# Kernel optimization log

Measured on AMD Instinct MI355X. Metric: run time of the kernel, lower is better.

Reference implementation:

```python
import jax, jax.numpy as jnp
import numpy as np

N, C, H, W = 8, 256, 128, 128
HW = H * W
NB = 20            # boxes per image
TEMP = 0.5
RATIO = 1.0
IMG_H, IMG_W = 800.0, 800.0  # img_metas[i]['img_shape']


def setup_inputs() -> dict:
    key = jax.random.key(0)
    k1, k2, k3 = jax.random.split(key, 3)
    preds_S = jax.random.normal(k1, (HW, N, C), dtype=jnp.float32)
    preds_T = jax.random.normal(k2, (HW, N, C), dtype=jnp.float32)
    # boxes: random corner pairs in image coords, sorted so x1<=x2, y1<=y2
    u = jax.random.uniform(k3, (N, NB, 4), dtype=jnp.float32)
    x1 = jnp.minimum(u[..., 0], u[..., 2]) * IMG_W
    x2 = jnp.maximum(u[..., 0], u[..., 2]) * IMG_W
    y1 = jnp.minimum(u[..., 1], u[..., 3]) * IMG_H
    y2 = jnp.maximum(u[..., 1], u[..., 3]) * IMG_H
    gt_bboxes = jnp.stack([x1, y1, x2, y2], axis=-1)  # (N, NB, 4)
    return {"preds_S": preds_S, "preds_T": preds_T, "gt_bboxes": gt_bboxes}


def get_attention(preds, temp):
    # preds: (N, C, H, W)
    value = jnp.abs(preds)
    fea_map = value.mean(axis=1)                                   # (N, H, W)
    S_att = (H * W) * jax.nn.softmax((fea_map / temp).reshape(N, -1), axis=1)
    S_att = S_att.reshape(N, H, W)
    channel_map = value.mean(axis=(2, 3))                          # (N, C)
    C_att = C * jax.nn.softmax(channel_map / temp, axis=1)
    return S_att, C_att


def build_masks(gt_bboxes):
    # boxes scaled to feature grid (same math as torch loop, vectorized)
    wmin = jnp.floor(gt_bboxes[..., 0] / IMG_W * W).astype(jnp.int32)  # (N, NB)
    wmax = jnp.ceil(gt_bboxes[..., 2] / IMG_W * W).astype(jnp.int32)
    hmin = jnp.floor(gt_bboxes[..., 1] / IMG_H * H).astype(jnp.int32)
    hmax = jnp.ceil(gt_bboxes[..., 3] / IMG_H * H).astype(jnp.int32)
    area = 1.0 / (hmax + 1 - hmin).astype(jnp.float32) / (wmax + 1 - wmin).astype(jnp.float32)
    hh = jnp.arange(H)[None, None, :, None]
    ww = jnp.arange(W)[None, None, None, :]
    inside = ((hh >= hmin[:, :, None, None]) & (hh <= hmax[:, :, None, None]) &
              (ww >= wmin[:, :, None, None]) & (ww <= wmax[:, :, None, None]))  # (N, NB, H, W)
    # per-box max-scatter == max over boxes of (area where inside else 0)
    Mask_fg = jnp.max(jnp.where(inside, area[:, :, None, None], 0.0), axis=1)  # (N, H, W)
    Mask_bg = (Mask_fg <= 0).astype(jnp.float32)
    s = Mask_bg.sum(axis=(1, 2), keepdims=True)
    Mask_bg = jnp.where(s > 0, Mask_bg / s, Mask_bg)
    return Mask_fg, Mask_bg


def reference(preds_S, preds_T, gt_bboxes):
    # attention from DETACHED teacher features (preds_T.detach() in torch)
    pT_det = jax.lax.stop_gradient(preds_T)
    pT_new = pT_det.reshape(H, W, N, C).transpose(2, 3, 0, 1)  # (N, C, H, W)
    S_t, C_t = get_attention(pT_new, TEMP)

    Mask_fg, Mask_bg = build_masks(gt_bboxes)

    # flatten to the (HW, bs, .) layout of get_fea_loss
    flat = lambda m: m.transpose(1, 2, 0).reshape(HW, N, 1)
    S_t_f = flat(S_t)
    Mfg_f = flat(Mask_fg)
    Mbg_f = flat(Mask_bg)
    C_t_f = C_t[None]  # (1, bs, c) broadcast

    w = jnp.sqrt(S_t_f) * jnp.sqrt(C_t_f)
    fea_t = preds_T * w
    fea_s = preds_S * w
    diff = jnp.abs(fea_s - fea_t)
    fg_loss = jnp.sum(diff * jnp.sqrt(Mfg_f)) / HW
    bg_loss = jnp.sum(diff * jnp.sqrt(Mbg_f)) / HW
    return (fg_loss + bg_loss) * RATIO
```

## Files before the change

### kernel.cpp

```cpp
#include <hip/hip_runtime.h>

#define N_   8
#define C_   256
#define H_   128
#define W_   128
#define HW_  16384
#define NB_  20
constexpr float TEMP  = 0.5f;
constexpr float IMG_W = 800.0f;
constexpr float IMG_H = 800.0f;

__device__ __forceinline__ float waveReduceSum(float v) {
    v += __shfl_xor(v, 32, 64);
    v += __shfl_xor(v, 16, 64);
    v += __shfl_xor(v, 8, 64);
    v += __shfl_xor(v, 4, 64);
    v += __shfl_xor(v, 2, 64);
    v += __shfl_xor(v, 1, 64);
    return v;
}

__global__ __launch_bounds__(256, 4) void k_stats(const float* __restrict__ pT,
                                                  float* __restrict__ chan_part,
                                                  float* __restrict__ fea_sum,
                                                  float* __restrict__ smax_part) {
    const int n     = blockIdx.x & 7;
    const int chunk = blockIdx.x >> 3;
    const int wave  = threadIdx.x >> 6;
    const int lane  = threadIdx.x & 63;
    const int hw0   = chunk * 64 + wave * 16;

    float4 cacc = make_float4(0.f, 0.f, 0.f, 0.f);
    float vmax = 0.f;
    #pragma unroll
    for (int g = 0; g < 4; ++g) {
        const int r = hw0 + g * 4;
        float p[4];
        #pragma unroll
        for (int j = 0; j < 4; ++j) {
            const float4 v = *(const float4*)(pT + ((size_t)((r + j) * N_ + n)) * C_ + lane * 4);
            const float ax = fabsf(v.x), ay = fabsf(v.y), az = fabsf(v.z), aw = fabsf(v.w);
            cacc.x += ax; cacc.y += ay; cacc.z += az; cacc.w += aw;
            p[j] = ax + ay + az + aw;
        }
        float a01 = (lane & 32) ? p[1] : p[0];
        float b01 = (lane & 32) ? p[0] : p[1];
        const float u01 = a01 + __shfl_xor(b01, 32, 64);
        float a23 = (lane & 32) ? p[3] : p[2];
        float b23 = (lane & 32) ? p[2] : p[3];
        const float u23 = a23 + __shfl_xor(b23, 32, 64);
        float aq = (lane & 16) ? u23 : u01;
        float bq = (lane & 16) ? u01 : u23;
        float u = aq + __shfl_xor(bq, 16, 64);
        u += __shfl_xor(u, 8, 64);
        u += __shfl_xor(u, 4, 64);
        u += __shfl_xor(u, 2, 64);
        u += __shfl_xor(u, 1, 64);
        vmax = fmaxf(vmax, u);
        if ((lane & 15) == 0) {
            const int q = lane >> 4;
            const int row = ((q & 1) << 1) | (q >> 1);
            fea_sum[n * HW_ + r + row] = u;
        }
    }
    vmax = fmaxf(vmax, __shfl_xor(vmax, 16, 64));
    vmax = fmaxf(vmax, __shfl_xor(vmax, 32, 64));

    __shared__ float lds[4][C_];
    __shared__ float wmax[4];
    if (lane == 0) wmax[wave] = vmax;
    ((float4*)lds[wave])[lane] = cacc;
    __syncthreads();
    const int c = threadIdx.x;
    chan_part[((size_t)(n * 256 + chunk)) * C_ + c] =
        lds[0][c] + lds[1][c] + lds[2][c] + lds[3][c];
    if (threadIdx.x == 0)
        smax_part[n * 256 + chunk] =
            fmaxf(fmaxf(wmax[0], wmax[1]), fmaxf(wmax[2], wmax[3]));
}

__global__ __launch_bounds__(256) void k_soft(const float* __restrict__ fea_sum,
                                              const float* __restrict__ chan_part,
                                              const float* __restrict__ smax_part,
                                              const float* __restrict__ gt,
                                              float* __restrict__ sden_part,
                                              float* __restrict__ bg_part,
                                              float* __restrict__ Mfg,
                                              float* __restrict__ stats,
                                              float* __restrict__ B) {
    const int n   = blockIdx.x >> 3;
    const int sub = blockIdx.x & 7;
    const int tid = threadIdx.x;
    __shared__ float red[256];

    red[tid] = smax_part[n * 256 + tid];
    __syncthreads();
    for (int s = 128; s > 0; s >>= 1) { if (tid < s) red[tid] = fmaxf(red[tid], red[tid + s]); __syncthreads(); }
    const float sm = red[0] * (1.0f / (C_ * TEMP));
    __syncthreads();

    float acc = 0.f;
    const int base = n * HW_ + sub * 2048;
    #pragma unroll
    for (int k = 0; k < 8; ++k)
        acc += expf(fea_sum[base + k * 256 + tid] * (1.0f / (C_ * TEMP)) - sm);
    red[tid] = acc; __syncthreads();
    for (int s = 128; s > 0; s >>= 1) { if (tid < s) red[tid] += red[tid + s]; __syncthreads(); }
    if (tid == 0) sden_part[n * 8 + sub] = red[0];
    __syncthreads();

    float fg[8] = {0.f, 0.f, 0.f, 0.f, 0.f, 0.f, 0.f, 0.f};
    for (int b = 0; b < NB_; ++b) {
        const float* bx = gt + ((size_t)n * NB_ + b) * 4;
        const float x1 = bx[0], y1 = bx[1], x2 = bx[2], y2 = bx[3];
        const int wmin = (int)floorf(x1 / IMG_W * (float)W_);
        const int wmax = (int)ceilf (x2 / IMG_W * (float)W_);
        const int hmin = (int)floorf(y1 / IMG_H * (float)H_);
        const int hmax = (int)ceilf (y2 / IMG_H * (float)H_);
        const float area = 1.0f / (float)(hmax + 1 - hmin) / (float)(wmax + 1 - wmin);
        #pragma unroll
        for (int k = 0; k < 8; ++k) {
            const int hw = sub * 2048 + k * 256 + tid;
            const int h = hw >> 7, w = hw & 127;
            if (h >= hmin && h <= hmax && w >= wmin && w <= wmax)
                fg[k] = fmaxf(fg[k], area);
        }
    }
    float bgc = 0.f;
    #pragma unroll
    for (int k = 0; k < 8; ++k) {
        const int hw = sub * 2048 + k * 256 + tid;
        Mfg[n * HW_ + hw] = fg[k];
        bgc += (fg[k] <= 0.f) ? 1.f : 0.f;
    }
    red[tid] = bgc; __syncthreads();
    for (int s = 128; s > 0; s >>= 1) { if (tid < s) red[tid] += red[tid + s]; __syncthreads(); }
    if (tid == 0) bg_part[n * 8 + sub] = red[0];
    if (tid == 0 && sub == 0) stats[n] = sm;

    if (sub != 0) return;
    __syncthreads();

    float cs = 0.f;
    #pragma unroll 4
    for (int k2 = 0; k2 < 256; ++k2)
        cs += chan_part[((size_t)(n * 256 + k2)) * C_ + tid];
    const float lc = cs * (1.0f / (HW_ * TEMP));
    red[tid] = lc; __syncthreads();
    for (int s = 128; s > 0; s >>= 1) { if (tid < s) red[tid] = fmaxf(red[tid], red[tid + s]); __syncthreads(); }
    const float cmax = red[0]; __syncthreads();
    const float e = expf(lc - cmax);
    red[tid] = e; __syncthreads();
    for (int s = 128; s > 0; s >>= 1) { if (tid < s) red[tid] += red[tid + s]; __syncthreads(); }
    B[n * C_ + tid] = sqrtf((float)C_ * e / red[0]);
}

__global__ __launch_bounds__(256, 4) void k_main(const float* __restrict__ pS,
                                                 const float* __restrict__ pT,
                                                 const float* __restrict__ fea_sum,
                                                 const float* __restrict__ Mfg,
                                                 const float* __restrict__ bg_part,
                                                 const float* __restrict__ stats,
                                                 const float* __restrict__ sden_part,
                                                 const float* __restrict__ B,
                                                 float* __restrict__ partials) {
    const int wave = threadIdx.x >> 6, lane = threadIdx.x & 63;
    const int wg   = blockIdx.x * 4 + wave;
    const int n    = wg & 7;
    const int widx = wg >> 3;
    const int hw0  = widx * 16;
    const float sm = stats[n];
    float sden = 0.f, bgs = 0.f;
    #pragma unroll
    for (int j = 0; j < 8; ++j) { sden += sden_part[n * 8 + j]; bgs += bg_part[n * 8 + j]; }
    const float bginv = (bgs > 0.f) ? 1.0f / bgs : 1.0f;
    const float4 B4 = *(const float4*)(B + n * C_ + lane * 4);
    float acc = 0.f;
    #pragma unroll 4
    for (int i = 0; i < 16; ++i) {
        const int hw = hw0 + i;
        const float fs = fea_sum[n * HW_ + hw];
        const float fg = Mfg[n * HW_ + hw];
        const float S_att = (float)HW_ * expf(fs * (1.0f / (C_ * TEMP)) - sm) / sden;
        const float bg = (fg <= 0.f) ? bginv : 0.f;
        const float a_row = sqrtf(S_att) * (sqrtf(fg) + sqrtf(bg)) * (1.0f / (float)HW_);
        const size_t off = ((size_t)(hw * N_ + n)) * C_ + lane * 4;
        const float4 sv = *(const float4*)(pS + off);
        const float4 tv = *(const float4*)(pT + off);
        const float part = fabsf(sv.x - tv.x) * B4.x + fabsf(sv.y - tv.y) * B4.y +
                           fabsf(sv.z - tv.z) * B4.z + fabsf(sv.w - tv.w) * B4.w;
        acc += a_row * part;
    }
    acc = waveReduceSum(acc);
    __shared__ float red[4];
    if (lane == 0) red[wave] = acc;
    __syncthreads();
    if (threadIdx.x == 0) partials[blockIdx.x] = red[0] + red[1] + red[2] + red[3];
}

__global__ __launch_bounds__(256) void k_final(const float* __restrict__ partials,
                                               float* __restrict__ out) {
    float a = 0.f;
    for (int i = threadIdx.x; i < 2048; i += 256) a += partials[i];
    __shared__ float red[256];
    red[threadIdx.x] = a; __syncthreads();
    for (int s = 128; s > 0; s >>= 1) { if (threadIdx.x < s) red[threadIdx.x] += red[threadIdx.x + s]; __syncthreads(); }
    if (threadIdx.x == 0) out[0] = red[0];
}

extern "C" void kernel_launch(void* const* d_in, const int* in_sizes, int n_in,
                              void* d_out, int out_size, void* d_ws, size_t ws_size,
                              hipStream_t stream) {
    const float* pS = (const float*)d_in[0];
    const float* pT = (const float*)d_in[1];
    const float* gt = (const float*)d_in[2];
    float* ws = (float*)d_ws;

    float* chan_part = ws;
    float* smax_part = chan_part + 524288;
    float* sden_part = smax_part + 2048;
    float* bg_part   = sden_part + 64;
    float* stats     = bg_part + 64;
    float* fea_sum   = ws + 528384;
    float* Mfg       = fea_sum + N_ * HW_;
    float* B         = Mfg + N_ * HW_;
    float* partials  = B + N_ * C_;

    k_stats<<<2048, 256, 0, stream>>>(pT, chan_part, fea_sum, smax_part);
    k_soft <<<64,   256, 0, stream>>>(fea_sum, chan_part, smax_part, gt,
                                      sden_part, bg_part, Mfg, stats, B);
    k_main <<<2048, 256, 0, stream>>>(pS, pT, fea_sum, Mfg, bg_part, stats,
                                      sden_part, B, partials);
    k_final<<<1,    256, 0, stream>>>(partials, (float*)d_out);
}
```

Before: 315.0 us.

## Batch loads up front in stats/main kernels and precompute per-row weights in new kernel

k_stats now issues all 16 float4 loads of teacher data before reducing them, which raises memory-level parallelism. A new k_A kernel precomputes the per-pixel weight (spatial attention times mask terms) into a workspace array. k_main then loads one weight per lane and broadcasts it with shuffles, and it issues 8 rows of student and teacher loads at a time. This removes exp/sqrt work from the bandwidth-bound main loop, at the cost of more registers, an extra small launch and an extra workspace buffer.

Result: no change. 315.6 us (+0.2%).

```diff
diff --git a/kernel.cpp b/kernel.cpp
--- a/kernel.cpp
+++ b/kernel.cpp
@@ -30,6 +30,11 @@
     const int lane  = threadIdx.x & 63;
     const int hw0   = chunk * 64 + wave * 16;
 
+    float4 v[16];
+    #pragma unroll
+    for (int j = 0; j < 16; ++j)
+        v[j] = *(const float4*)(pT + ((size_t)((hw0 + j) * N_ + n)) * C_ + lane * 4);
+
     float4 cacc = make_float4(0.f, 0.f, 0.f, 0.f);
     float vmax = 0.f;
     #pragma unroll
@@ -38,8 +43,8 @@
         float p[4];
         #pragma unroll
         for (int j = 0; j < 4; ++j) {
-            const float4 v = *(const float4*)(pT + ((size_t)((r + j) * N_ + n)) * C_ + lane * 4);
-            const float ax = fabsf(v.x), ay = fabsf(v.y), az = fabsf(v.z), aw = fabsf(v.w);
+            const float4 w = v[g * 4 + j];
+            const float ax = fabsf(w.x), ay = fabsf(w.y), az = fabsf(w.z), aw = fabsf(w.w);
             cacc.x += ax; cacc.y += ay; cacc.z += az; cacc.w += aw;
             p[j] = ax + ay + az + aw;
         }
@@ -155,41 +160,58 @@
     B[n * C_ + tid] = sqrtf((float)C_ * e / red[0]);
 }
 
+__global__ __launch_bounds__(256) void k_A(const float* __restrict__ fea_sum,
+                                           const float* __restrict__ Mfg,
+                                           const float* __restrict__ sden_part,
+                                           const float* __restrict__ bg_part,
+                                           const float* __restrict__ stats,
+                                           float* __restrict__ A) {
+    const int n   = blockIdx.x >> 3;
+    const int sub = blockIdx.x & 7;
+    const int tid = threadIdx.x;
+    const float sm = stats[n];
+    float sden = 0.f, bgs = 0.f;
+    #pragma unroll
+    for (int j = 0; j < 8; ++j) { sden += sden_part[n * 8 + j]; bgs += bg_part[n * 8 + j]; }
+    const float bginv = (bgs > 0.f) ? 1.0f / bgs : 1.0f;
+    #pragma unroll
+    for (int k = 0; k < 8; ++k) {
+        const int hw = sub * 2048 + k * 256 + tid;
+        const float fs = fea_sum[n * HW_ + hw];
+        const float fg = Mfg[n * HW_ + hw];
+        const float S_att = (float)HW_ * expf(fs * (1.0f / (C_ * TEMP)) - sm) / sden;
+        const float bg = (fg <= 0.f) ? bginv : 0.f;
+        A[n * HW_ + hw] = sqrtf(S_att) * (sqrtf(fg) + sqrtf(bg)) * (1.0f / (float)HW_);
+    }
+}
+
 __global__ __launch_bounds__(256, 4) void k_main(const float* __restrict__ pS,
                                                  const float* __restrict__ pT,
-                                                 const float* __restrict__ fea_sum,
-                                                 const float* __restrict__ Mfg,
-                                                 const float* __restrict__ bg_part,
-                                                 const float* __restrict__ stats,
-                                                 const float* __restrict__ sden_part,
+                                                 const float* __restrict__ A,
                                                  const float* __restrict__ B,
                                                  float* __restrict__ partials) {
     const int wave = threadIdx.x >> 6, lane = threadIdx.x & 63;
     const int wg   = blockIdx.x * 4 + wave;
     const int n    = wg & 7;
-    const int widx = wg >> 3;
-    const int hw0  = widx * 16;
-    const float sm = stats[n];
-    float sden = 0.f, bgs = 0.f;
-    #pragma unroll
-    for (int j = 0; j < 8; ++j) { sden += sden_part[n * 8 + j]; bgs += bg_part[n * 8 + j]; }
-    const float bginv = (bgs > 0.f) ? 1.0f / bgs : 1.0f;
+    const int hw0  = (wg >> 3) * 16;
     const float4 B4 = *(const float4*)(B + n * C_ + lane * 4);
+    const float aval = A[n * HW_ + hw0 + (lane & 15)];
     float acc = 0.f;
-    #pragma unroll 4
-    for (int i = 0; i < 16; ++i) {
-        const int hw = hw0 + i;
-        const float fs = fea_sum[n * HW_ + hw];
-        const float fg = Mfg[n * HW_ + hw];
-        const float S_att = (float)HW_ * expf(fs * (1.0f / (C_ * TEMP)) - sm) / sden;
-        const float bg = (fg <= 0.f) ? bginv : 0.f;
-        const float a_row = sqrtf(S_att) * (sqrtf(fg) + sqrtf(bg)) * (1.0f / (float)HW_);
-        const size_t off = ((size_t)(hw * N_ + n)) * C_ + lane * 4;
-        const float4 sv = *(const float4*)(pS + off);
-        const float4 tv = *(const float4*)(pT + off);
-        const float part = fabsf(sv.x - tv.x) * B4.x + fabsf(sv.y - tv.y) * B4.y +
-                           fabsf(sv.z - tv.z) * B4.z + fabsf(sv.w - tv.w) * B4.w;
-        acc += a_row * part;
+    #pragma unroll
+    for (int half = 0; half < 2; ++half) {
+        float4 sv[8], tv[8];
+        #pragma unroll
+        for (int j = 0; j < 8; ++j) {
+            const size_t off = ((size_t)((hw0 + half * 8 + j) * N_ + n)) * C_ + lane * 4;
+            sv[j] = *(const float4*)(pS + off);
+            tv[j] = *(const float4*)(pT + off);
+        }
+        #pragma unroll
+        for (int j = 0; j < 8; ++j) {
+            const float part = fabsf(sv[j].x - tv[j].x) * B4.x + fabsf(sv[j].y - tv[j].y) * B4.y +
+                               fabsf(sv[j].z - tv[j].z) * B4.z + fabsf(sv[j].w - tv[j].w) * B4.w;
+            acc += __shfl(aval, half * 8 + j, 64) * part;
+        }
     }
     acc = waveReduceSum(acc);
     __shared__ float red[4];
@@ -223,13 +245,14 @@
     float* stats     = bg_part + 64;
     float* fea_sum   = ws + 528384;
     float* Mfg       = fea_sum + N_ * HW_;
-    float* B         = Mfg + N_ * HW_;
+    float* A         = Mfg + N_ * HW_;
+    float* B         = A + N_ * HW_;
     float* partials  = B + N_ * C_;
 
     k_stats<<<2048, 256, 0, stream>>>(pT, chan_part, fea_sum, smax_part);
     k_soft <<<64,   256, 0, stream>>>(fea_sum, chan_part, smax_part, gt,
                                       sden_part, bg_part, Mfg, stats, B);
-    k_main <<<2048, 256, 0, stream>>>(pS, pT, fea_sum, Mfg, bg_part, stats,
-                                      sden_part, B, partials);
+    k_A    <<<64,   256, 0, stream>>>(fea_sum, Mfg, sden_part, bg_part, stats, A);
+    k_main <<<2048, 256, 0, stream>>>(pS, pT, A, B, partials);
     k_final<<<1,    256, 0, stream>>>(partials, (float*)d_out);
 }
```

## Precompute per-row attention weights in prep kernel and restructure main streaming kernel

Applied to the files above, without the earlier changes.

The prep kernel now computes the full spatial softmax denominator and background count per image redundantly in every block. It then writes a combined per-(hw,n) weight A_t laid out hw-major, so the main kernel no longer recomputes exp/sqrt per row. The main kernel assigns one wave per spatial position covering all 8 images, preloads B into LDS, issues 16 float4 loads up front (nontemporal for pS) and doubles the grid. This trades redundant reductions in the small prep kernel for fewer per-row transcendental ops and more memory-level parallelism in the bandwidth-bound main pass.

Measured after the change: 384.7 us. 22.1% more time.

```diff
diff --git a/kernel.cpp b/kernel.cpp
--- a/kernel.cpp
+++ b/kernel.cpp
@@ -9,6 +9,8 @@
 constexpr float TEMP  = 0.5f;
 constexpr float IMG_W = 800.0f;
 constexpr float IMG_H = 800.0f;
+
+using f4 = __attribute__((ext_vector_type(4))) float;
 
 __device__ __forceinline__ float waveReduceSum(float v) {
     v += __shfl_xor(v, 32, 64);
@@ -79,19 +81,28 @@
             fmaxf(fmaxf(wmax[0], wmax[1]), fmaxf(wmax[2], wmax[3]));
 }
 
-__global__ __launch_bounds__(256) void k_soft(const float* __restrict__ fea_sum,
+__global__ __launch_bounds__(256) void k_prep(const float* __restrict__ fea_sum,
                                               const float* __restrict__ chan_part,
                                               const float* __restrict__ smax_part,
                                               const float* __restrict__ gt,
-                                              float* __restrict__ sden_part,
-                                              float* __restrict__ bg_part,
-                                              float* __restrict__ Mfg,
-                                              float* __restrict__ stats,
+                                              float* __restrict__ A_t,
                                               float* __restrict__ B) {
     const int n   = blockIdx.x >> 3;
     const int sub = blockIdx.x & 7;
     const int tid = threadIdx.x;
     __shared__ float red[256];
+    __shared__ int   bb[NB_][4];
+    __shared__ float barea[NB_];
+
+    if (tid < NB_) {
+        const float* bx = gt + ((size_t)n * NB_ + tid) * 4;
+        const int wmin = (int)floorf(bx[0] / IMG_W * (float)W_);
+        const int wmax = (int)ceilf (bx[2] / IMG_W * (float)W_);
+        const int hmin = (int)floorf(bx[1] / IMG_H * (float)H_);
+        const int hmax = (int)ceilf (bx[3] / IMG_H * (float)H_);
+        bb[tid][0] = wmin; bb[tid][1] = wmax; bb[tid][2] = hmin; bb[tid][3] = hmax;
+        barea[tid] = 1.0f / (float)(hmax + 1 - hmin) / (float)(wmax + 1 - wmin);
+    }
 
     red[tid] = smax_part[n * 256 + tid];
     __syncthreads();
@@ -100,43 +111,38 @@
     __syncthreads();
 
     float acc = 0.f;
-    const int base = n * HW_ + sub * 2048;
-    #pragma unroll
-    for (int k = 0; k < 8; ++k)
-        acc += expf(fea_sum[base + k * 256 + tid] * (1.0f / (C_ * TEMP)) - sm);
+    for (int i = tid; i < HW_; i += 256)
+        acc += expf(fea_sum[n * HW_ + i] * (1.0f / (C_ * TEMP)) - sm);
     red[tid] = acc; __syncthreads();
     for (int s = 128; s > 0; s >>= 1) { if (tid < s) red[tid] += red[tid + s]; __syncthreads(); }
-    if (tid == 0) sden_part[n * 8 + sub] = red[0];
-    __syncthreads();
-
-    float fg[8] = {0.f, 0.f, 0.f, 0.f, 0.f, 0.f, 0.f, 0.f};
-    for (int b = 0; b < NB_; ++b) {
-        const float* bx = gt + ((size_t)n * NB_ + b) * 4;
-        const float x1 = bx[0], y1 = bx[1], x2 = bx[2], y2 = bx[3];
-        const int wmin = (int)floorf(x1 / IMG_W * (float)W_);
-        const int wmax = (int)ceilf (x2 / IMG_W * (float)W_);
-        const int hmin = (int)floorf(y1 / IMG_H * (float)H_);
-        const int hmax = (int)ceilf (y2 / IMG_H * (float)H_);
-        const float area = 1.0f / (float)(hmax + 1 - hmin) / (float)(wmax + 1 - wmin);
-        #pragma unroll
-        for (int k = 0; k < 8; ++k) {
-            const int hw = sub * 2048 + k * 256 + tid;
-            const int h = hw >> 7, w = hw & 127;
-            if (h >= hmin && h <= hmax && w >= wmin && w <= wmax)
-                fg[k] = fmaxf(fg[k], area);
-        }
-    }
-    float bgc = 0.f;
-    #pragma unroll
+    const float sden = red[0];
+    __syncthreads();
+
+    float cnt = 0.f;
+    for (int i = tid; i < HW_; i += 256) {
+        const int h = i >> 7, w = i & 127;
+        bool in = false;
+        for (int b = 0; b < NB_; ++b)
+            in = in || (h >= bb[b][2] && h <= bb[b][3] && w >= bb[b][0] && w <= bb[b][1]);
+        cnt += in ? 0.f : 1.f;
+    }
+    red[tid] = cnt; __syncthreads();
+    for (int s = 128; s > 0; s >>= 1) { if (tid < s) red[tid] += red[tid + s]; __syncthreads(); }
+    const float bgs = red[0];
+    const float bginv = (bgs > 0.f) ? 1.0f / bgs : 1.0f;
+    __syncthreads();
+
     for (int k = 0; k < 8; ++k) {
-        const int hw = sub * 2048 + k * 256 + tid;
-        Mfg[n * HW_ + hw] = fg[k];
-        bgc += (fg[k] <= 0.f) ? 1.f : 0.f;
-    }
-    red[tid] = bgc; __syncthreads();
-    for (int s = 128; s > 0; s >>= 1) { if (tid < s) red[tid] += red[tid + s]; __syncthreads(); }
-    if (tid == 0) bg_part[n * 8 + sub] = red[0];
-    if (tid == 0 && sub == 0) stats[n] = sm;
+        const int i = sub * 2048 + k * 256 + tid;
+        const int h = i >> 7, w = i & 127;
+        float fg = 0.f;
+        for (int b = 0; b < NB_; ++b)
+            if (h >= bb[b][2] && h <= bb[b][3] && w >= bb[b][0] && w <= bb[b][1])
+                fg = fmaxf(fg, barea[b]);
+        const float S_att = (float)HW_ * expf(fea_sum[n * HW_ + i] * (1.0f / (C_ * TEMP)) - sm) / sden;
+        const float bg = (fg <= 0.f) ? bginv : 0.f;
+        A_t[(size_t)i * 8 + n] = sqrtf(S_att) * (sqrtf(fg) + sqrtf(bg)) * (1.0f / (float)HW_);
+    }
 
     if (sub != 0) return;
     __syncthreads();
@@ -157,51 +163,47 @@
 
 __global__ __launch_bounds__(256, 4) void k_main(const float* __restrict__ pS,
                                                  const float* __restrict__ pT,
-                                                 const float* __restrict__ fea_sum,
-                                                 const float* __restrict__ Mfg,
-                                                 const float* __restrict__ bg_part,
-                                                 const float* __restrict__ stats,
-                                                 const float* __restrict__ sden_part,
+                                                 const float* __restrict__ A_t,
                                                  const float* __restrict__ B,
                                                  float* __restrict__ partials) {
-    const int wave = threadIdx.x >> 6, lane = threadIdx.x & 63;
-    const int wg   = blockIdx.x * 4 + wave;
-    const int n    = wg & 7;
-    const int widx = wg >> 3;
-    const int hw0  = widx * 16;
-    const float sm = stats[n];
-    float sden = 0.f, bgs = 0.f;
-    #pragma unroll
-    for (int j = 0; j < 8; ++j) { sden += sden_part[n * 8 + j]; bgs += bg_part[n * 8 + j]; }
-    const float bginv = (bgs > 0.f) ? 1.0f / bgs : 1.0f;
-    const float4 B4 = *(const float4*)(B + n * C_ + lane * 4);
+    __shared__ float4 ldsB[512];
+    const int tid = threadIdx.x;
+    ldsB[tid]       = ((const float4*)B)[tid];
+    ldsB[tid + 256] = ((const float4*)B)[tid + 256];
+    __syncthreads();
+
+    const int wave = tid >> 6, lane = tid & 63;
+    const int hw   = blockIdx.x * 4 + wave;
+    float a[8];
+    #pragma unroll
+    for (int j = 0; j < 8; ++j) a[j] = A_t[(size_t)hw * 8 + j];
+
+    const size_t base4 = (size_t)hw * 512 + lane;
+    f4 sv[8], tv[8];
+    #pragma unroll
+    for (int j = 0; j < 8; ++j) {
+        sv[j] = __builtin_nontemporal_load((const f4*)pS + base4 + (size_t)j * 64);
+        tv[j] = *((const f4*)pT + base4 + (size_t)j * 64);
+    }
     float acc = 0.f;
-    #pragma unroll 4
-    for (int i = 0; i < 16; ++i) {
-        const int hw = hw0 + i;
-        const float fs = fea_sum[n * HW_ + hw];
-        const float fg = Mfg[n * HW_ + hw];
-        const float S_att = (float)HW_ * expf(fs * (1.0f / (C_ * TEMP)) - sm) / sden;
-        const float bg = (fg <= 0.f) ? bginv : 0.f;
-        const float a_row = sqrtf(S_att) * (sqrtf(fg) + sqrtf(bg)) * (1.0f / (float)HW_);
-        const size_t off = ((size_t)(hw * N_ + n)) * C_ + lane * 4;
-        const float4 sv = *(const float4*)(pS + off);
-        const float4 tv = *(const float4*)(pT + off);
-        const float part = fabsf(sv.x - tv.x) * B4.x + fabsf(sv.y - tv.y) * B4.y +
-                           fabsf(sv.z - tv.z) * B4.z + fabsf(sv.w - tv.w) * B4.w;
-        acc += a_row * part;
+    #pragma unroll
+    for (int j = 0; j < 8; ++j) {
+        const float4 b4 = ldsB[j * 64 + lane];
+        const float part = fabsf(sv[j].x - tv[j].x) * b4.x + fabsf(sv[j].y - tv[j].y) * b4.y +
+                           fabsf(sv[j].z - tv[j].z) * b4.z + fabsf(sv[j].w - tv[j].w) * b4.w;
+        acc += a[j] * part;
     }
     acc = waveReduceSum(acc);
     __shared__ float red[4];
     if (lane == 0) red[wave] = acc;
     __syncthreads();
-    if (threadIdx.x == 0) partials[blockIdx.x] = red[0] + red[1] + red[2] + red[3];
+    if (tid == 0) partials[blockIdx.x] = red[0] + red[1] + red[2] + red[3];
 }
 
 __global__ __launch_bounds__(256) void k_final(const float* __restrict__ partials,
                                                float* __restrict__ out) {
     float a = 0.f;
-    for (int i = threadIdx.x; i < 2048; i += 256) a += partials[i];
+    for (int i = threadIdx.x; i < 4096; i += 256) a += partials[i];
     __shared__ float red[256];
     red[threadIdx.x] = a; __syncthreads();
     for (int s = 128; s > 0; s >>= 1) { if (threadIdx.x < s) red[threadIdx.x] += red[threadIdx.x + s]; __syncthreads(); }
@@ -218,18 +220,13 @@
 
     float* chan_part = ws;
     float* smax_part = chan_part + 524288;
-    float* sden_part = smax_part + 2048;
-    float* bg_part   = sden_part + 64;
-    float* stats     = bg_part + 64;
-    float* fea_sum   = ws + 528384;
-    float* Mfg       = fea_sum + N_ * HW_;
-    float* B         = Mfg + N_ * HW_;
-    float* partials  = B + N_ * C_;
+    float* fea_sum   = smax_part + 2048;
+    float* A_t       = fea_sum + 131072;
+    float* B         = A_t + 131072;
+    float* partials  = B + 2048;
 
     k_stats<<<2048, 256, 0, stream>>>(pT, chan_part, fea_sum, smax_part);
-    k_soft <<<64,   256, 0, stream>>>(fea_sum, chan_part, smax_part, gt,
-                                      sden_part, bg_part, Mfg, stats, B);
-    k_main <<<2048, 256, 0, stream>>>(pS, pT, fea_sum, Mfg, bg_part, stats,
-                                      sden_part, B, partials);
+    k_prep <<<64,   256, 0, stream>>>(fea_sum, chan_part, smax_part, gt, A_t, B);
+    k_main <<<4096, 256, 0, stream>>>(pS, pT, A_t, B, partials);
     k_final<<<1,    256, 0, stream>>>(partials, (float*)d_out);
 }
```
